# Kernel optimization log

Measured on AMD Instinct MI355X. Metric: run time of the kernel, lower is better.

## Reference

```python
import jax, jax.numpy as jnp
import numpy as np

B, L = 2, 2048
IN_DIM, HD_DIM, STATE_DIM = 512, 4096, 16
NUM_PATHS, ENT_DEPTH = 2, 2
ENT_STRENGTH, WALK_TIME = 0.3, 1.0


def _glorot(key, shape):
    lim = np.sqrt(6.0 / (shape[0] + shape[1]))
    return jax.random.uniform(key, shape, jnp.float32, -lim, lim)


def setup_inputs() -> dict:
    key = jax.random.key(0)
    ks = jax.random.split(key, 10)
    x = jax.random.normal(ks[0], (B, L, IN_DIM), jnp.float32)
    input_proj = _glorot(ks[1], (IN_DIM, HD_DIM))
    output_proj = _glorot(ks[2], (HD_DIM, IN_DIM))
    a_log = jax.random.uniform(ks[3], (STATE_DIM,), jnp.float32, -4.0, -1.0)
    b_proj = _glorot(ks[4], (HD_DIM, STATE_DIM))
    c_proj = _glorot(ks[5], (HD_DIM, STATE_DIM))
    dt_proj = jnp.full((HD_DIM,), 0.01, jnp.float32)
    skip_proj = jnp.ones((HD_DIM,), jnp.float32)  # diagonal skip, init 1.0
    amplitudes_real = jnp.full((NUM_PATHS,), 1.0 / np.sqrt(NUM_PATHS), jnp.float32)
    amplitudes_imag = 0.01 * jax.random.normal(ks[6], (NUM_PATHS,), jnp.float32)
    rotation_angles = jax.random.uniform(ks[7], (ENT_DEPTH, NUM_PATHS), jnp.float32, 0.0, 2.0 * np.pi)
    wh, _ = jnp.linalg.qr(jax.random.normal(ks[8], (NUM_PATHS, NUM_PATHS), jnp.float32))  # orthogonal init
    return dict(x=x, input_proj=input_proj, output_proj=output_proj, a_log=a_log,
                b_proj=b_proj, c_proj=c_proj, dt_proj=dt_proj, skip_proj=skip_proj,
                amplitudes_real=amplitudes_real, amplitudes_imag=amplitudes_imag,
                rotation_angles=rotation_angles, walk_hamiltonian=wh)


def _qhd_forward(x, input_proj, output_proj, a_log, b_proj, c_proj, dt_proj,
                 skip_proj, amp_r, amp_i, rot, walk_h):
    Bb, Ll, _ = x.shape
    K = amp_r.shape[0]
    dt = jax.nn.softplus(dt_proj)                                   # (D,)
    hd = jnp.einsum('bld,dh->blh', x, input_proj)                   # (B,L,D)
    # --- frequency-stratified superposition paths (K bands) ---
    Xf = jnp.fft.rfft(hd, axis=1)                                   # (B,F,D) complex
    F = Xf.shape[1]
    band = jnp.clip(jnp.arange(F) * K // F, 0, K - 1)
    masks = (band[None, :] == jnp.arange(K)[:, None]).astype(hd.dtype)  # (K,F)
    x_paths = jnp.fft.irfft(Xf[None] * masks[:, None, :, None], n=Ll, axis=2)  # (K,B,L,D)
    # --- FFT-domain diagonal selective SSM (causal conv with exp decay) ---
    a = -jnp.exp(a_log)                                             # (N,)
    dt_bar = jnp.mean(dt)
    t_idx = jnp.arange(Ll, dtype=hd.dtype)
    decay = jnp.exp(a[None, :] * dt_bar * t_idx[:, None])           # (L,N)
    Bt = jnp.einsum('kbld,dn->kbln', x_paths * dt, b_proj)          # (K,B,L,N)
    n2 = 2 * Ll
    h = jnp.fft.irfft(jnp.fft.rfft(Bt, n=n2, axis=2) * jnp.fft.rfft(decay, n=n2, axis=0),
                      n=n2, axis=2)[:, :, :Ll, :]                   # (K,B,L,N)
    y_paths = jnp.einsum('kbln,dn->kbld', h, c_proj)                # (K,B,L,D)
    # --- VQC entanglement (RY-style phase + quantum-walk mixing) ---
    alpha = amp_r.astype(jnp.complex64) + 1j * amp_i.astype(jnp.complex64)
    A = 1j * (ENT_STRENGTH * WALK_TIME) * walk_h.astype(jnp.complex64)
    U = jnp.eye(K, dtype=jnp.complex64) + A + (A @ A) / 2.0 + (A @ A @ A) / 6.0
    for d in range(rot.shape[0]):
        alpha = jnp.exp(1j * rot[d].astype(jnp.complex64)) * alpha
        alpha = U @ alpha
    # --- Born rule collapse ---
    w = jnp.abs(alpha) ** 2
    w = (w / jnp.sum(w)).astype(hd.dtype)                           # (K,)
    y = jnp.einsum('k,kbld->bld', w, y_paths) + hd * skip_proj      # diagonal skip
    return jnp.einsum('blh,hd->bld', y, output_proj)                # (B,L,in_dim)


def reference(x, input_proj, output_proj, a_log, b_proj, c_proj, dt_proj,
              skip_proj, amplitudes_real, amplitudes_imag, rotation_angles,
              walk_hamiltonian):
    return _qhd_forward(x, input_proj, output_proj, a_log, b_proj, c_proj,
                        dt_proj, skip_proj, amplitudes_real, amplitudes_imag,
                        rotation_angles, walk_hamiltonian)
```

## Files before the change

### kernel.cpp

```cpp
#include <hip/hip_runtime.h>
#include <cstdint>

typedef unsigned short ushort_t;
typedef __bf16 bf16x8 __attribute__((ext_vector_type(8)));
typedef float f32x4 __attribute__((ext_vector_type(4)));

#define PI_F 3.14159265358979323846f

__device__ __forceinline__ ushort_t f2bf(float f) {
  uint32_t x = __float_as_uint(f);
  x += 0x7fffu + ((x >> 16) & 1u);
  return (ushort_t)(x >> 16);
}
__device__ __forceinline__ float bf2f(ushort_t u) {
  return __uint_as_float(((uint32_t)u) << 16);
}
__device__ __forceinline__ float softplusf(float x) {
  return (x > 20.f) ? x : log1pf(expf(x));
}
__device__ __forceinline__ void async_ld16(ushort_t* lds, const ushort_t* g) {
  __builtin_amdgcn_global_load_lds(
      (const __attribute__((address_space(1))) uint32_t*)g,
      (__attribute__((address_space(3))) uint32_t*)lds, 16, 0, 0);
}
__device__ __forceinline__ void load16f(const float* p, float* v) {
  const float4* q = reinterpret_cast<const float4*>(p);
  float4 t0 = q[0], t1 = q[1], t2 = q[2], t3 = q[3];
  v[0]=t0.x; v[1]=t0.y; v[2]=t0.z; v[3]=t0.w;
  v[4]=t1.x; v[5]=t1.y; v[6]=t1.z; v[7]=t1.w;
  v[8]=t2.x; v[9]=t2.y; v[10]=t2.z; v[11]=t2.w;
  v[12]=t3.x; v[13]=t3.y; v[14]=t3.z; v[15]=t3.w;
}


__global__ __launch_bounds__(256) void cast_bf16(const float* __restrict__ in,
                                                 ushort_t* __restrict__ out, int n) {
  int i = blockIdx.x * 256 + threadIdx.x;
  if (i < n) out[i] = f2bf(in[i]);
}

__global__ __launch_bounds__(256) void transpose_cast(const float* __restrict__ in,
                                                      ushort_t* __restrict__ out,
                                                      int R, int C) {
  __shared__ float t[32][33];
  int bc = blockIdx.x * 32;
  int br = blockIdx.y * 32;
  int tx = threadIdx.x, ty = threadIdx.y;
#pragma unroll
  for (int i = ty; i < 32; i += 8)
    t[i][tx] = in[(size_t)(br + i) * C + bc + tx];
  __syncthreads();
#pragma unroll
  for (int i = ty; i < 32; i += 8)
    out[(size_t)(bc + i) * R + br + tx] = f2bf(t[tx][i]);
}

__global__ __launch_bounds__(256) void bdt_kernel(const float* __restrict__ bp,
                                                  const float* __restrict__ dtp,
                                                  float* __restrict__ bdt) {
  int i = blockIdx.x * 256 + threadIdx.x;
  bdt[i] = bp[i] * softplusf(dtp[i >> 4]);
}

__global__ __launch_bounds__(256) void small_setup(const float* __restrict__ dtp,
                                                   const float* __restrict__ a_log,
                                                   const float* __restrict__ ar,
                                                   const float* __restrict__ ai,
                                                   const float* __restrict__ rot,
                                                   const float* __restrict__ wh,
                                                   float* __restrict__ sc) {
  __shared__ float red[256];
  float s = 0.f;
  for (int i = threadIdx.x; i < 4096; i += 256) s += softplusf(dtp[i]);
  red[threadIdx.x] = s;
  __syncthreads();
  for (int st = 128; st > 0; st >>= 1) {
    if (threadIdx.x < st) red[threadIdx.x] += red[threadIdx.x + st];
    __syncthreads();
  }
  if (threadIdx.x == 0) {
    float dtbar = red[0] / 4096.f;
    float B00 = 0.3f * wh[0], B01 = 0.3f * wh[1], B10 = 0.3f * wh[2], B11 = 0.3f * wh[3];
    float C00 = B00*B00 + B01*B10, C01 = B00*B01 + B01*B11;
    float C10 = B10*B00 + B11*B10, C11 = B10*B01 + B11*B11;
    float D00 = C00*B00 + C01*B10, D01 = C00*B01 + C01*B11;
    float D10 = C10*B00 + C11*B10, D11 = C10*B01 + C11*B11;
    float Ur00 = 1.f - 0.5f*C00, Ur01 = -0.5f*C01, Ur10 = -0.5f*C10, Ur11 = 1.f - 0.5f*C11;
    float Ui00 = B00 - D00/6.f, Ui01 = B01 - D01/6.f, Ui10 = B10 - D10/6.f, Ui11 = B11 - D11/6.f;
    float a0r = ar[0], a0i = ai[0], a1r = ar[1], a1i = ai[1];
#pragma unroll
    for (int d = 0; d < 2; ++d) {
      float c0 = cosf(rot[d*2+0]), s0 = sinf(rot[d*2+0]);
      float c1 = cosf(rot[d*2+1]), s1 = sinf(rot[d*2+1]);
      float t0r = a0r*c0 - a0i*s0, t0i = a0r*s0 + a0i*c0;
      float t1r = a1r*c1 - a1i*s1, t1i = a1r*s1 + a1i*c1;
      a0r = Ur00*t0r - Ui00*t0i + Ur01*t1r - Ui01*t1i;
      a0i = Ur00*t0i + Ui00*t0r + Ur01*t1i + Ui01*t1r;
      a1r = Ur10*t0r - Ui10*t0i + Ur11*t1r - Ui11*t1i;
      a1i = Ur10*t0i + Ui10*t0r + Ur11*t1i + Ui11*t1r;
    }
    float p0 = a0r*a0r + a0i*a0i, p1 = a1r*a1r + a1i*a1i;
    float inv = 1.f / (p0 + p1);
    sc[0] = p0 * inv; sc[1] = p1 * inv; sc[2] = dtbar;
#pragma unroll
    for (int n = 0; n < 16; ++n) {
      float a = -expf(a_log[n]);
      sc[8 + n]  = expf(a * dtbar);
      sc[24 + n] = expf(a * dtbar * 32.f);
    }
  }
}


__global__ __launch_bounds__(256)
void skinny16(const float* __restrict__ A, const float* __restrict__ Bm,
              float* __restrict__ C, int K, int lda) {
  const int m0 = blockIdx.x << 2;
  const int tid = threadIdx.x;
  float acc[4][16];
#pragma unroll
  for (int a = 0; a < 4; ++a)
#pragma unroll
    for (int n = 0; n < 16; ++n) acc[a][n] = 0.f;

  for (int d = tid; d < K; d += 256) {
    float bv[16];
    load16f(Bm + (size_t)d * 16, bv);
    float av[4];
#pragma unroll
    for (int a = 0; a < 4; ++a) av[a] = A[(size_t)(m0 + a) * lda + d];
#pragma unroll
    for (int a = 0; a < 4; ++a)
#pragma unroll
      for (int n = 0; n < 16; ++n) acc[a][n] += av[a] * bv[n];
  }
  __shared__ float sred[4][4][16];
  const int w = tid >> 6, lane = tid & 63;
#pragma unroll
  for (int a = 0; a < 4; ++a)
#pragma unroll
    for (int n = 0; n < 16; ++n) {
      float v = acc[a][n];
#pragma unroll
      for (int off2 = 32; off2 > 0; off2 >>= 1) v += __shfl_down(v, off2);
      if (lane == 0) sred[w][a][n] = v;
    }
  __syncthreads();
  if (tid < 64) {
    int a = tid >> 4, n = tid & 15;
    C[(size_t)(m0 + a) * 16 + n] =
        sred[0][a][n] + sred[1][a][n] + sred[2][a][n] + sred[3][a][n];
  }
}


template<int BM, int BN, int WR, int WC, bool OBF, bool FUSE>
__global__ __launch_bounds__(256)
void gemm_bf16(const ushort_t* __restrict__ A, const ushort_t* __restrict__ Bt,
               void* __restrict__ Cv, int M, int N, int Kc, int lda, int ldb, int swz,
               const float* __restrict__ hvp, const float* __restrict__ cj,
               const float* __restrict__ skp) {
  constexpr int BK = 64;
  constexpr int WMR = BM / WR;
  constexpr int WNC = BN / WC;
  constexpr int MI = WMR / 16;
  constexpr int NI = WNC / 16;
  constexpr int NCA = BM * BK * 2 / 1024;
  constexpr int NCB = BN * BK * 2 / 1024;

  __shared__ ushort_t lA[BM * BK];
  __shared__ ushort_t lB[BN * BK];

  const int tid = threadIdx.x;
  const int w = tid >> 6, lane = tid & 63;
  const int wr = w / WC, wc = w % WC;
  const int r = lane & 15, g = lane >> 4;

  const int nbx = gridDim.x;
  int bid = blockIdx.y * nbx + blockIdx.x;
  if (swz) {
    const int nwg = nbx * gridDim.y;
    bid = (bid & 7) * (nwg >> 3) + (bid >> 3);
  }
  const int m0 = (bid / nbx) * BM, n0 = (bid % nbx) * BN;
  const int kz = blockIdx.z * Kc;

  f32x4 acc[MI][NI];
#pragma unroll
  for (int mi = 0; mi < MI; ++mi)
#pragma unroll
    for (int ni = 0; ni < NI; ++ni)
      acc[mi][ni] = (f32x4){0.f, 0.f, 0.f, 0.f};

  const int ktiles = Kc >> 6;
  for (int kt = 0; kt < ktiles; ++kt) {
    const int k0 = kz + (kt << 6);
    for (int c = w; c < NCA; c += 4) {
      int byteoff = (c << 10) + (lane << 4);
      int row = byteoff >> 7;
      int scol = (byteoff & 127) ^ ((row & 7) << 4);
      async_ld16(&lA[c << 9], &A[(size_t)(m0 + row) * lda + k0 + (scol >> 1)]);
    }
    for (int c = w; c < NCB; c += 4) {
      int byteoff = (c << 10) + (lane << 4);
      int row = byteoff >> 7;
      int scol = (byteoff & 127) ^ ((row & 7) << 4);
      async_ld16(&lB[c << 9], &Bt[(size_t)(n0 + row) * ldb + k0 + (scol >> 1)]);
    }
    __syncthreads();
#pragma unroll
    for (int kk = 0; kk < 2; ++kk) {
      bf16x8 av[MI], bv[NI];
#pragma unroll
      for (int mi = 0; mi < MI; ++mi) {
        int row = wr * WMR + mi * 16 + r;
        int off = (((kk << 2) + g) ^ (row & 7)) << 3;
        av[mi] = *reinterpret_cast<const bf16x8*>(&lA[row * 64 + off]);
      }
#pragma unroll
      for (int ni = 0; ni < NI; ++ni) {
        int row = wc * WNC + ni * 16 + r;
        int off = (((kk << 2) + g) ^ (row & 7)) << 3;
        bv[ni] = *reinterpret_cast<const bf16x8*>(&lB[row * 64 + off]);
      }
#pragma unroll
      for (int mi = 0; mi < MI; ++mi)
#pragma unroll
        for (int ni = 0; ni < NI; ++ni)
          acc[mi][ni] = __builtin_amdgcn_mfma_f32_16x16x32_bf16(av[mi], bv[ni], acc[mi][ni], 0, 0, 0);
    }
    __syncthreads();
  }

  if constexpr (FUSE) {
    float* hsh = reinterpret_cast<float*>(lA);
    {
      const float4* src = reinterpret_cast<const float4*>(hvp + (size_t)m0 * 16);
      float4* dst = reinterpret_cast<float4*>(hsh);
      for (int q = tid; q < BM * 4; q += 256) dst[q] = src[q];
    }
    float cr[NI][16];
    float skv[NI];
    int colg[NI];
#pragma unroll
    for (int ni = 0; ni < NI; ++ni) {
      colg[ni] = n0 + wc * WNC + ni * 16 + r;
      load16f(cj + (size_t)colg[ni] * 16, cr[ni]);
      skv[ni] = skp[colg[ni]];
    }
    __syncthreads();
#pragma unroll
    for (int mi = 0; mi < MI; ++mi)
#pragma unroll
      for (int j = 0; j < 4; ++j) {
        int row_l = wr * WMR + mi * 16 + g * 4 + j;
        float hr[16];
        load16f(hsh + row_l * 16, hr);
#pragma unroll
        for (int ni = 0; ni < NI; ++ni) {
          float v = acc[mi][ni][j] * skv[ni];
#pragma unroll
          for (int n = 0; n < 16; ++n) v += cr[ni][n] * hr[n];
          ((ushort_t*)Cv)[(size_t)(m0 + row_l) * N + colg[ni]] = f2bf(v);
        }
      }
  } else {
    const size_t zoff = (size_t)blockIdx.z * (size_t)M * (size_t)N;
#pragma unroll
    for (int mi = 0; mi < MI; ++mi)
#pragma unroll
      for (int ni = 0; ni < NI; ++ni) {
        int row = m0 + wr * WMR + mi * 16 + g * 4;
        int col = n0 + wc * WNC + ni * 16 + r;
#pragma unroll
        for (int j = 0; j < 4; ++j) {
          size_t idx = zoff + (size_t)(row + j) * N + col;
          if (OBF) ((ushort_t*)Cv)[idx] = f2bf(acc[mi][ni][j]);
          else     ((float*)Cv)[idx]   = acc[mi][ni][j];
        }
      }
  }
}


__global__ __launch_bounds__(256)
void reduceK(const float4* __restrict__ p, float4* __restrict__ out) {
  int i = blockIdx.x * 256 + threadIdx.x;
  float4 a = p[i];
  float4 b = p[i + 524288];
  float4 c = p[i + 1048576];
  float4 d = p[i + 1572864];
  float4 o;
  o.x = a.x + b.x + c.x + d.x;
  o.y = a.y + b.y + c.y + d.y;
  o.z = a.z + b.z + c.z + d.z;
  o.w = a.w + b.w + c.w + d.w;
  out[i] = o;
}


__global__ __launch_bounds__(256)
void freq_ssm(const float* __restrict__ Bhd, const float* __restrict__ sc,
              float* __restrict__ h) {
  const int blk = blockIdx.x;
  const int b = blk >> 4, n = blk & 15;
  const int tid = threadIdx.x;
  __shared__ float2 X[2048];
  __shared__ float carr[64], pre[64];
  const float w0 = sc[0], w1 = sc[1];
  const float r = sc[8 + n], r32 = sc[24 + n];

  for (int l = tid; l < 2048; l += 256) {
    X[l].x = Bhd[(size_t)(b * 2048 + l) * 16 + n];
    X[l].y = 0.f;
  }
  for (int ls = 10; ls >= 0; --ls) {
    int s = 1 << ls;
    __syncthreads();
    for (int q = tid; q < 1024; q += 256) {
      int j = q & (s - 1);
      int base = (q >> ls) << (ls + 1);
      int i0 = base + j, i1 = i0 + s;
      float2 a = X[i0], bb = X[i1];
      X[i0].x = a.x + bb.x; X[i0].y = a.y + bb.y;
      float tx = a.x - bb.x, ty = a.y - bb.y;
      float ang = -PI_F * (float)j / (float)s;
      float sn, cs; sincosf(ang, &sn, &cs);
      X[i1].x = tx * cs - ty * sn;
      X[i1].y = tx * sn + ty * cs;
    }
  }
  __syncthreads();
  for (int i = tid; i < 2048; i += 256) {
    unsigned f = __brev((unsigned)i) >> 21;
    float wv = (f <= 512u || f >= 1536u) ? w0 : w1;
    X[i].x *= wv; X[i].y *= wv;
  }
  for (int ls = 0; ls <= 10; ++ls) {
    int s = 1 << ls;
    __syncthreads();
    for (int q = tid; q < 1024; q += 256) {
      int j = q & (s - 1);
      int base = (q >> ls) << (ls + 1);
      int i0 = base + j, i1 = i0 + s;
      float ang = PI_F * (float)j / (float)s;
      float sn, cs; sincosf(ang, &sn, &cs);
      float2 bb = X[i1];
      float bx = bb.x * cs - bb.y * sn;
      float by = bb.x * sn + bb.y * cs;
      float2 a = X[i0];
      X[i0].x = a.x + bx; X[i0].y = a.y + by;
      X[i1].x = a.x - bx; X[i1].y = a.y - by;
    }
  }
  __syncthreads();
  const float inv = 1.0f / 2048.0f;
  if (tid < 64) {
    float c = 0.f;
    int base = tid * 32;
#pragma unroll
    for (int i = 0; i < 32; ++i) c = r * c + X[base + i].x * inv;
    carr[tid] = c;
  }
  __syncthreads();
  if (tid == 0) {
    float s = 0.f;
    for (int j2 = 0; j2 < 64; ++j2) { pre[j2] = s; s = s * r32 + carr[j2]; }
  }
  __syncthreads();
  if (tid < 64) {
    float s = pre[tid];
    int base = tid * 32;
#pragma unroll
    for (int i = 0; i < 32; ++i) {
      s = r * s + X[base + i].x * inv;
      h[(size_t)(b * 2048 + base + i) * 16 + n] = s;
    }
  }
}


extern "C" void kernel_launch(void* const* d_in, const int* in_sizes, int n_in,
                              void* d_out, int out_size, void* d_ws, size_t ws_size,
                              hipStream_t stream) {
  (void)in_sizes; (void)n_in; (void)out_size; (void)ws_size;
  const float* x      = (const float*)d_in[0];
  const float* Win    = (const float*)d_in[1];
  const float* Wout   = (const float*)d_in[2];
  const float* a_log  = (const float*)d_in[3];
  const float* b_proj = (const float*)d_in[4];
  const float* c_proj = (const float*)d_in[5];
  const float* dt_proj= (const float*)d_in[6];
  const float* skip   = (const float*)d_in[7];
  const float* ampr   = (const float*)d_in[8];
  const float* ampi   = (const float*)d_in[9];
  const float* rot    = (const float*)d_in[10];
  const float* wh     = (const float*)d_in[11];
  float* out = (float*)d_out;

  char* ws = (char*)d_ws;
  ushort_t* A1  = (ushort_t*)(ws + 0);
  ushort_t* Wt1 = (ushort_t*)(ws + 4194304);
  ushort_t* Wt2 = (ushort_t*)(ws + 8388608);
  float*    bdt = (float*)(ws + 12582912);
  float*    Wb  = (float*)(ws + 12845056);
  float*    Bhd = (float*)(ws + 12910592);
  float*    hv  = (float*)(ws + 13172736);
  float*    sc  = (float*)(ws + 13434880);
  ushort_t* y   = (ushort_t*)(ws + 13435136);
  float*    part= (float*)(ws + 46989568);

  cast_bf16<<<8192, 256, 0, stream>>>(x, A1, 4096 * 512);
  transpose_cast<<<dim3(128, 16), dim3(32, 8), 0, stream>>>(Win, Wt1, 512, 4096);
  transpose_cast<<<dim3(16, 128), dim3(32, 8), 0, stream>>>(Wout, Wt2, 4096, 512);
  bdt_kernel<<<256, 256, 0, stream>>>(b_proj, dt_proj, bdt);
  small_setup<<<1, 256, 0, stream>>>(dt_proj, a_log, ampr, ampi, rot, wh, sc);

  skinny16<<<128, 256, 0, stream>>>(Win, bdt, Wb, 4096, 4096);
  skinny16<<<1024, 256, 0, stream>>>(x, Wb, Bhd, 512, 512);
  freq_ssm<<<32, 256, 0, stream>>>(Bhd, sc, hv);

  gemm_bf16<128, 128, 2, 2, true, true><<<dim3(32, 32), 256, 0, stream>>>(
      A1, Wt1, y, 4096, 4096, 512, 512, 512, 1, hv, c_proj, skip);

  gemm_bf16<64, 128, 1, 4, false, false><<<dim3(4, 64, 4), 256, 0, stream>>>(
      y, Wt2, part, 4096, 512, 1024, 4096, 4096, 1, nullptr, nullptr, nullptr);
  reduceK<<<2048, 256, 0, stream>>>((const float4*)part, (float4*)out);
}
```

Baseline: 253.7 us.

## Fold rank-16 epilogue into MFMA, fold skip into weights, atomic split-K output

New measurement: 261.6 us. +3.1%, slower.

```diff
diff --git a/kernel.cpp b/kernel.cpp
--- a/kernel.cpp
+++ b/kernel.cpp
@@ -39,9 +39,15 @@
   if (i < n) out[i] = f2bf(in[i]);
 }
 
+__global__ __launch_bounds__(256) void zero_f4(float4* __restrict__ p) {
+  int i = blockIdx.x * 256 + threadIdx.x;
+  p[i] = (float4){0.f, 0.f, 0.f, 0.f};
+}
+
 __global__ __launch_bounds__(256) void transpose_cast(const float* __restrict__ in,
                                                       ushort_t* __restrict__ out,
-                                                      int R, int C) {
+                                                      int R, int C,
+                                                      const float* __restrict__ scale) {
   __shared__ float t[32][33];
   int bc = blockIdx.x * 32;
   int br = blockIdx.y * 32;
@@ -51,8 +57,10 @@
     t[i][tx] = in[(size_t)(br + i) * C + bc + tx];
   __syncthreads();
 #pragma unroll
-  for (int i = ty; i < 32; i += 8)
-    out[(size_t)(bc + i) * R + br + tx] = f2bf(t[tx][i]);
+  for (int i = ty; i < 32; i += 8) {
+    float sv = scale ? scale[bc + i] : 1.f;
+    out[(size_t)(bc + i) * R + br + tx] = f2bf(t[tx][i] * sv);
+  }
 }
 
 __global__ __launch_bounds__(256) void bdt_kernel(const float* __restrict__ bp,
@@ -158,8 +166,7 @@
 __global__ __launch_bounds__(256)
 void gemm_bf16(const ushort_t* __restrict__ A, const ushort_t* __restrict__ Bt,
                void* __restrict__ Cv, int M, int N, int Kc, int lda, int ldb, int swz,
-               const float* __restrict__ hvp, const float* __restrict__ cj,
-               const float* __restrict__ skp) {
+               const ushort_t* __restrict__ hb, const ushort_t* __restrict__ cp) {
   constexpr int BK = 64;
   constexpr int WMR = BM / WR;
   constexpr int WNC = BN / WC;
@@ -233,75 +240,52 @@
   }
 
   if constexpr (FUSE) {
-    float* hsh = reinterpret_cast<float*>(lA);
-    {
-      const float4* src = reinterpret_cast<const float4*>(hvp + (size_t)m0 * 16);
-      float4* dst = reinterpret_cast<float4*>(hsh);
-      for (int q = tid; q < BM * 4; q += 256) dst[q] = src[q];
-    }
-    float cr[NI][16];
-    float skv[NI];
-    int colg[NI];
+    bf16x8 zv;
+#pragma unroll
+    for (int t2 = 0; t2 < 8; ++t2) zv[t2] = (__bf16)0.0f;
+    bf16x8 ah[MI], bh[NI];
+#pragma unroll
+    for (int mi = 0; mi < MI; ++mi) {
+      ah[mi] = zv;
+      if (g < 2) {
+        int row = m0 + wr * WMR + mi * 16 + r;
+        ah[mi] = *reinterpret_cast<const bf16x8*>(&hb[(size_t)row * 16 + g * 8]);
+      }
+    }
 #pragma unroll
     for (int ni = 0; ni < NI; ++ni) {
-      colg[ni] = n0 + wc * WNC + ni * 16 + r;
-      load16f(cj + (size_t)colg[ni] * 16, cr[ni]);
-      skv[ni] = skp[colg[ni]];
-    }
-    __syncthreads();
+      bh[ni] = zv;
+      if (g < 2) {
+        int col = n0 + wc * WNC + ni * 16 + r;
+        bh[ni] = *reinterpret_cast<const bf16x8*>(&cp[(size_t)col * 16 + g * 8]);
+      }
+    }
 #pragma unroll
     for (int mi = 0; mi < MI; ++mi)
 #pragma unroll
+      for (int ni = 0; ni < NI; ++ni)
+        acc[mi][ni] = __builtin_amdgcn_mfma_f32_16x16x32_bf16(ah[mi], bh[ni], acc[mi][ni], 0, 0, 0);
+  }
+
+#pragma unroll
+  for (int mi = 0; mi < MI; ++mi)
+#pragma unroll
+    for (int ni = 0; ni < NI; ++ni) {
+      int row = m0 + wr * WMR + mi * 16 + g * 4;
+      int col = n0 + wc * WNC + ni * 16 + r;
+#pragma unroll
       for (int j = 0; j < 4; ++j) {
-        int row_l = wr * WMR + mi * 16 + g * 4 + j;
-        float hr[16];
-        load16f(hsh + row_l * 16, hr);
-#pragma unroll
-        for (int ni = 0; ni < NI; ++ni) {
-          float v = acc[mi][ni][j] * skv[ni];
-#pragma unroll
-          for (int n = 0; n < 16; ++n) v += cr[ni][n] * hr[n];
-          ((ushort_t*)Cv)[(size_t)(m0 + row_l) * N + colg[ni]] = f2bf(v);
-        }
+        size_t idx = (size_t)(row + j) * N + col;
+        if (OBF) ((ushort_t*)Cv)[idx] = f2bf(acc[mi][ni][j]);
+        else     unsafeAtomicAdd(&((float*)Cv)[idx], acc[mi][ni][j]);
       }
-  } else {
-    const size_t zoff = (size_t)blockIdx.z * (size_t)M * (size_t)N;
-#pragma unroll
-    for (int mi = 0; mi < MI; ++mi)
-#pragma unroll
-      for (int ni = 0; ni < NI; ++ni) {
-        int row = m0 + wr * WMR + mi * 16 + g * 4;
-        int col = n0 + wc * WNC + ni * 16 + r;
-#pragma unroll
-        for (int j = 0; j < 4; ++j) {
-          size_t idx = zoff + (size_t)(row + j) * N + col;
-          if (OBF) ((ushort_t*)Cv)[idx] = f2bf(acc[mi][ni][j]);
-          else     ((float*)Cv)[idx]   = acc[mi][ni][j];
-        }
-      }
-  }
-}
-
-
-__global__ __launch_bounds__(256)
-void reduceK(const float4* __restrict__ p, float4* __restrict__ out) {
-  int i = blockIdx.x * 256 + threadIdx.x;
-  float4 a = p[i];
-  float4 b = p[i + 524288];
-  float4 c = p[i + 1048576];
-  float4 d = p[i + 1572864];
-  float4 o;
-  o.x = a.x + b.x + c.x + d.x;
-  o.y = a.y + b.y + c.y + d.y;
-  o.z = a.z + b.z + c.z + d.z;
-  o.w = a.w + b.w + c.w + d.w;
-  out[i] = o;
+    }
 }
 
 
 __global__ __launch_bounds__(256)
 void freq_ssm(const float* __restrict__ Bhd, const float* __restrict__ sc,
-              float* __restrict__ h) {
+              ushort_t* __restrict__ h) {
   const int blk = blockIdx.x;
   const int b = blk >> 4, n = blk & 15;
   const int tid = threadIdx.x;
@@ -374,7 +358,7 @@
 #pragma unroll
     for (int i = 0; i < 32; ++i) {
       s = r * s + X[base + i].x * inv;
-      h[(size_t)(b * 2048 + base + i) * 16 + n] = s;
+      h[(size_t)(b * 2048 + base + i) * 16 + n] = f2bf(s);
     }
   }
 }
@@ -405,25 +389,26 @@
   float*    bdt = (float*)(ws + 12582912);
   float*    Wb  = (float*)(ws + 12845056);
   float*    Bhd = (float*)(ws + 12910592);
-  float*    hv  = (float*)(ws + 13172736);
+  ushort_t* hb  = (ushort_t*)(ws + 13172736);
+  ushort_t* cp16= (ushort_t*)(ws + 13303808);
   float*    sc  = (float*)(ws + 13434880);
   ushort_t* y   = (ushort_t*)(ws + 13435136);
-  float*    part= (float*)(ws + 46989568);
-
+
+  zero_f4<<<2048, 256, 0, stream>>>((float4*)out);
   cast_bf16<<<8192, 256, 0, stream>>>(x, A1, 4096 * 512);
-  transpose_cast<<<dim3(128, 16), dim3(32, 8), 0, stream>>>(Win, Wt1, 512, 4096);
-  transpose_cast<<<dim3(16, 128), dim3(32, 8), 0, stream>>>(Wout, Wt2, 4096, 512);
+  cast_bf16<<<256, 256, 0, stream>>>(c_proj, cp16, 65536);
+  transpose_cast<<<dim3(128, 16), dim3(32, 8), 0, stream>>>(Win, Wt1, 512, 4096, skip);
+  transpose_cast<<<dim3(16, 128), dim3(32, 8), 0, stream>>>(Wout, Wt2, 4096, 512, nullptr);
   bdt_kernel<<<256, 256, 0, stream>>>(b_proj, dt_proj, bdt);
   small_setup<<<1, 256, 0, stream>>>(dt_proj, a_log, ampr, ampi, rot, wh, sc);
 
   skinny16<<<128, 256, 0, stream>>>(Win, bdt, Wb, 4096, 4096);
   skinny16<<<1024, 256, 0, stream>>>(x, Wb, Bhd, 512, 512);
-  freq_ssm<<<32, 256, 0, stream>>>(Bhd, sc, hv);
+  freq_ssm<<<32, 256, 0, stream>>>(Bhd, sc, hb);
 
   gemm_bf16<128, 128, 2, 2, true, true><<<dim3(32, 32), 256, 0, stream>>>(
-      A1, Wt1, y, 4096, 4096, 512, 512, 512, 1, hv, c_proj, skip);
+      A1, Wt1, y, 4096, 4096, 512, 512, 512, 1, hb, cp16);
 
   gemm_bf16<64, 128, 1, 4, false, false><<<dim3(4, 64, 4), 256, 0, stream>>>(
-      y, Wt2, part, 4096, 512, 1024, 4096, 4096, 1, nullptr, nullptr, nullptr);
-  reduceK<<<2048, 256, 0, stream>>>((const float4*)part, (float4*)out);
-}
+      y, Wt2, out, 4096, 512, 1024, 4096, 4096, 1, nullptr, nullptr);
+}
```
